# Kernel tuning notes

Hardware: AMD Instinct MI355X
Metric: run time of the kernel (lower is better)

The kernel has to match this reference:

```python
import jax, jax.numpy as jnp
import numpy as np

DIM = 128
HEADS = 4
HD = DIM // HEADS  # 32
WS = 8             # search window (ws x ws candidates)
K = 16             # top-k neighbors kept
SCALE = HD ** -0.5


def _sepconv(x, w_dw, w_pw, b):
    # depthwise 3x3 ('SAME', reflect-free) + pointwise 1x1 with bias (SepConv2d)
    C = x.shape[1]
    y = jax.lax.conv_general_dilated(x, w_dw, (1, 1), 'SAME',
                                     feature_group_count=C,
                                     dimension_numbers=('NCHW', 'OIHW', 'NCHW'))
    return jnp.einsum('bchw,oc->bohw', y, w_pw) + b[None, :, None, None]


def _refl(i, n):
    # dnls reflect_bounds: mirror indices back into [0, n-1]
    i = jnp.where(i < 0, -i, i)
    return jnp.where(i >= n, 2 * (n - 1) - i, i)


def _neighbor_idx(T, H, W, ws):
    # flat pixel index of the ws*ws spatial candidates per query (wt=0: same frame)
    off = jnp.arange(ws) - ws // 2
    ni = _refl(jnp.arange(H)[:, None] + off[None, :], H)  # [H,ws]
    nj = _refl(jnp.arange(W)[:, None] + off[None, :], W)  # [W,ws]
    pix = ni[:, None, :, None] * W + nj[None, :, None, :]  # [H,W,ws,ws]
    idx = jnp.arange(T)[:, None, None, None, None] * (H * W) + pix[None]
    return idx.reshape(T * H * W, ws * ws).astype(jnp.int32)  # [Q,L]


def reference(vid, wq_dw, wq_pw, bq, wk_dw, wk_pw, bk, wv_dw, wv_pw, bv, proj_w, proj_b):
    B, T, C, H, W = vid.shape
    Q = T * H * W
    x = vid.reshape(B * T, C, H, W)
    # qkv conv projection; q pre-scaled as in get_qkv
    q = _sepconv(x, wq_dw, wq_pw, bq) * SCALE
    k = _sepconv(x, wk_dw, wk_pw, bk)
    v = _sepconv(x, wv_dw, wv_pw, bv)

    def heads(z):  # [B*T,C,H,W] -> [B,heads,Q,hd]
        return z.reshape(B, T, HEADS, HD, H, W).transpose(0, 2, 1, 4, 5, 3).reshape(B, HEADS, Q, HD)

    qh, kh, vh = heads(q), heads(k), heads(v)
    idx = _neighbor_idx(T, H, W, WS)            # [Q,L]
    kg = jnp.take(kh, idx, axis=2)              # [B,h,Q,L,hd] irregular gather
    dists = jnp.einsum('bhqd,bhqld->bhql', qh, kg)
    vals, args = jax.lax.top_k(dists, K)        # k-NN by prod distance
    attn = jax.nn.softmax(vals, axis=-1)        # run_softmax over k
    sel = jnp.take_along_axis(jnp.broadcast_to(idx[None, None], (B, HEADS) + idx.shape), args, axis=-1)
    vsel = jnp.take_along_axis(vh, sel.reshape(B, HEADS, Q * K)[..., None], axis=2).reshape(B, HEADS, Q, K, HD)
    out = jnp.einsum('bhqk,bhqkd->bhqd', attn, vsel)   # wpsum (ps=pt=1)
    out = out.transpose(0, 2, 1, 3).reshape(B, Q, C)   # merge heads: (h c)
    y = out @ proj_w.T + proj_b                        # nn.Linear proj
    # fold: ps=1, stride0=1 -> zvid==1, pure reshape back to video
    return y.reshape(B, T, H, W, C).transpose(0, 1, 4, 2, 3)


def setup_inputs() -> dict:
    key = jax.random.key(0)
    ks = jax.random.split(key, 12)
    s = 0.02
    return {
        'vid': jax.random.normal(ks[0], (1, 2, DIM, 96, 96), jnp.float32),
        'wq_dw': jax.random.normal(ks[1], (DIM, 1, 3, 3), jnp.float32) * s,
        'wq_pw': jax.random.normal(ks[2], (DIM, DIM), jnp.float32) * s,
        'bq': jax.random.normal(ks[3], (DIM,), jnp.float32) * s,
        'wk_dw': jax.random.normal(ks[4], (DIM, 1, 3, 3), jnp.float32) * s,
        'wk_pw': jax.random.normal(ks[5], (DIM, DIM), jnp.float32) * s,
        'bk': jax.random.normal(ks[6], (DIM,), jnp.float32) * s,
        'wv_dw': jax.random.normal(ks[7], (DIM, 1, 3, 3), jnp.float32) * s,
        'wv_pw': jax.random.normal(ks[8], (DIM, DIM), jnp.float32) * s,
        'bv': jax.random.normal(ks[9], (DIM,), jnp.float32) * s,
        'proj_w': jax.random.normal(ks[10], (DIM, DIM), jnp.float32) * s,
        'proj_b': jax.random.normal(ks[11], (DIM,), jnp.float32) * s,
    }
```

## Files before the change

kernel.cpp:

```cpp
#include <hip/hip_runtime.h>
#include <math.h>

#define TT 2
#define CH 128
#define HH 96
#define WW 96
#define HWS 9216
#define QTOT 18432
#define QC (QTOT*CH)
#define HD 32
#define KTOP 16
#define SCALE 0.17677669529663687f

#define SEG 16
#define PR 8
#define PC 23
#define PSTRIDE 36

#define WB_TOT 98304

typedef __attribute__((ext_vector_type(8))) short short8;
typedef __attribute__((ext_vector_type(4))) float floatx4;

__device__ __forceinline__ unsigned short f2bf(float f) {
    union { float f; unsigned u; } x; x.f = f;
    unsigned r = x.u + 0x7fffu + ((x.u >> 16) & 1u);
    return (unsigned short)(r >> 16);
}
__device__ __forceinline__ float bf2f(unsigned short h) {
    return __uint_as_float(((unsigned)h) << 16);
}

__device__ __forceinline__ int refl(int x, int n) {
    x = x < 0 ? -x : x;
    return x >= n ? 2 * (n - 1) - x : x;
}

__global__ __launch_bounds__(256) void dwcvt_kernel(
    const float* __restrict__ x,
    const float* __restrict__ wq, const float* __restrict__ wk, const float* __restrict__ wv,
    const float* __restrict__ wq_pw, const float* __restrict__ wk_pw,
    const float* __restrict__ wv_pw, const float* __restrict__ proj_w,
    unsigned short* __restrict__ qk_hi,
    unsigned short* __restrict__ qk_lo,
    unsigned short* __restrict__ v_bf,
    unsigned short* __restrict__ wbuf)
{
    int t = threadIdx.x;
    if (blockIdx.x == 288) {
        int y = blockIdx.y;
        const float* src = y == 0 ? wq_pw : (y == 1 ? wk_pw : (y == 2 ? wv_pw : proj_w));
        unsigned short* hi = wbuf + (y == 0 ? 0 : (y == 1 ? 32768 : (y == 2 ? 65536 : 81920)));
#pragma unroll
        for (int r = 0; r < 16; r++) {
            int idx = r * 256 + t;
            float4 w4 = *(const float4*)(src + idx * 4);
            unsigned short hx = f2bf(w4.x), hy = f2bf(w4.y), hz = f2bf(w4.z), hw = f2bf(w4.w);
            uint2 pk;
            pk.x = hx | ((unsigned)hy << 16); pk.y = hz | ((unsigned)hw << 16);
            *(uint2*)(hi + idx * 4) = pk;
            if (y < 2) {
                unsigned short lx = f2bf(w4.x - bf2f(hx)), ly = f2bf(w4.y - bf2f(hy));
                unsigned short lz = f2bf(w4.z - bf2f(hz)), lw = f2bf(w4.w - bf2f(hw));
                pk.x = lx | ((unsigned)ly << 16); pk.y = lz | ((unsigned)lw << 16);
                *(uint2*)(hi + 16384 + idx * 4) = pk;
            }
        }
        return;
    }

    int pl = t & 63;
    int cg = __builtin_amdgcn_readfirstlane(t >> 6);
    int p  = blockIdx.x * 64 + pl;
    int c0 = blockIdx.y * 32 + cg * 8;
    int hw = p % HWS;
    int tt = p / HWS;
    int i = hw / WW, j = hw % WW;

    unsigned qh[4], ql[4], kh[4], kl[4], vh4[4];
#pragma unroll
    for (int ic = 0; ic < 8; ic += 2) {
        float sv[3][2];
#pragma unroll
        for (int u = 0; u < 2; u++) {
            int c = c0 + ic + u;
            const float* xp = x + (size_t)(tt * CH + c) * HWS;
            float w0[9], w1[9], w2[9];
#pragma unroll
            for (int r = 0; r < 9; r++) {
                w0[r] = wq[c * 9 + r]; w1[r] = wk[c * 9 + r]; w2[r] = wv[c * 9 + r];
            }
            float s0 = 0.f, s1 = 0.f, s2 = 0.f;
#pragma unroll
            for (int r = 0; r < 3; r++) {
                int ii = i + r - 1;
                if (ii < 0 || ii >= HH) continue;
#pragma unroll
                for (int ss = 0; ss < 3; ss++) {
                    int jj = j + ss - 1;
                    if (jj < 0 || jj >= WW) continue;
                    float xv = xp[ii * WW + jj];
                    s0 += xv * w0[r * 3 + ss];
                    s1 += xv * w1[r * 3 + ss];
                    s2 += xv * w2[r * 3 + ss];
                }
            }
            sv[0][u] = s0; sv[1][u] = s1; sv[2][u] = s2;
        }
        int w = ic >> 1;
        unsigned short h0 = f2bf(sv[0][0]), h1 = f2bf(sv[0][1]);
        qh[w] = h0 | ((unsigned)h1 << 16);
        ql[w] = f2bf(sv[0][0] - bf2f(h0)) | ((unsigned)f2bf(sv[0][1] - bf2f(h1)) << 16);
        h0 = f2bf(sv[1][0]); h1 = f2bf(sv[1][1]);
        kh[w] = h0 | ((unsigned)h1 << 16);
        kl[w] = f2bf(sv[1][0] - bf2f(h0)) | ((unsigned)f2bf(sv[1][1] - bf2f(h1)) << 16);
        vh4[w] = f2bf(sv[2][0]) | ((unsigned)f2bf(sv[2][1]) << 16);
    }
    size_t off = (size_t)p * CH + c0;
    uint4 pk;
    pk.x = qh[0]; pk.y = qh[1]; pk.z = qh[2]; pk.w = qh[3];
    *(uint4*)(qk_hi + off) = pk;
    pk.x = ql[0]; pk.y = ql[1]; pk.z = ql[2]; pk.w = ql[3];
    *(uint4*)(qk_lo + off) = pk;
    pk.x = kh[0]; pk.y = kh[1]; pk.z = kh[2]; pk.w = kh[3];
    *(uint4*)(qk_hi + (size_t)QC + off) = pk;
    pk.x = kl[0]; pk.y = kl[1]; pk.z = kl[2]; pk.w = kl[3];
    *(uint4*)(qk_lo + (size_t)QC + off) = pk;
    pk.x = vh4[0]; pk.y = vh4[1]; pk.z = vh4[2]; pk.w = vh4[3];
    *(uint4*)(v_bf + off) = pk;
}

__global__ __launch_bounds__(256) void qkv_mfma(
    const unsigned short* __restrict__ Ahi,
    const unsigned short* __restrict__ Alo,
    const unsigned short* __restrict__ Avb,
    const unsigned short* __restrict__ wbuf,
    const float* __restrict__ bq, const float* __restrict__ bk, const float* __restrict__ bv,
    float* __restrict__ qkf,
    unsigned short* __restrict__ vh)
{
    int sel = blockIdx.y;
    int t = threadIdx.x;
    int wv = t >> 6, lane = t & 63;
    int m = lane & 15, quad = lane >> 4;
    int p0 = blockIdx.x * 64;
    int o0 = wv * 32;

    if (sel == 2) {
        const unsigned short* Wg = wbuf + 65536;
        float bb[2];
#pragma unroll
        for (int ot = 0; ot < 2; ot++) bb[ot] = bv[o0 + ot * 16 + m];
        floatx4 acc[4][2];
#pragma unroll
        for (int i = 0; i < 4; i++)
#pragma unroll
            for (int j = 0; j < 2; j++) acc[i][j] = (floatx4){0.f, 0.f, 0.f, 0.f};
#pragma unroll
        for (int kc = 0; kc < 4; kc++) {
            short8 a[4], b[2];
#pragma unroll
            for (int pt = 0; pt < 4; pt++)
                a[pt] = *(const short8*)(Avb + (size_t)(p0 + pt * 16 + m) * CH + kc * 32 + quad * 8);
#pragma unroll
            for (int ot = 0; ot < 2; ot++)
                b[ot] = *(const short8*)(Wg + (size_t)(o0 + ot * 16 + m) * CH + kc * 32 + quad * 8);
#pragma unroll
            for (int pt = 0; pt < 4; pt++)
#pragma unroll
                for (int ot = 0; ot < 2; ot++)
                    acc[pt][ot] = __builtin_amdgcn_mfma_f32_16x16x32_bf16(a[pt], b[ot], acc[pt][ot], 0, 0, 0);
        }
        unsigned short* vhh = vh + (size_t)wv * QTOT * 32;
#pragma unroll
        for (int pt = 0; pt < 4; pt++)
#pragma unroll
            for (int ot = 0; ot < 2; ot++)
#pragma unroll
                for (int reg = 0; reg < 4; reg++) {
                    int p = p0 + pt * 16 + quad * 4 + reg;
                    vhh[(size_t)p * 32 + ot * 16 + m] = f2bf(acc[pt][ot][reg] + bb[ot]);
                }
        return;
    }

    const unsigned short* Wh_g = wbuf + sel * 32768;
    const unsigned short* Wl_g = Wh_g + 16384;
    const float* bias = sel ? bk : bq;
    float scale = sel ? 1.f : SCALE;
    const unsigned short* ah = Ahi + (size_t)sel * QC;
    const unsigned short* al = Alo + (size_t)sel * QC;
    float* O = qkf + (size_t)sel * QC;

    float bb[2];
#pragma unroll
    for (int ot = 0; ot < 2; ot++) bb[ot] = bias[o0 + ot * 16 + m];
    floatx4 acc[4][2];
#pragma unroll
    for (int i = 0; i < 4; i++)
#pragma unroll
        for (int j = 0; j < 2; j++) acc[i][j] = (floatx4){0.f, 0.f, 0.f, 0.f};
#pragma unroll
    for (int kc = 0; kc < 4; kc++) {
        short8 avh[4], avl[4], bh[2], bl[2];
#pragma unroll
        for (int pt = 0; pt < 4; pt++) {
            size_t base = (size_t)(p0 + pt * 16 + m) * CH + kc * 32 + quad * 8;
            avh[pt] = *(const short8*)(ah + base);
            avl[pt] = *(const short8*)(al + base);
        }
#pragma unroll
        for (int ot = 0; ot < 2; ot++) {
            size_t widx = (size_t)(o0 + ot * 16 + m) * CH + kc * 32 + quad * 8;
            bh[ot] = *(const short8*)(Wh_g + widx);
            bl[ot] = *(const short8*)(Wl_g + widx);
        }
#pragma unroll
        for (int pt = 0; pt < 4; pt++)
#pragma unroll
            for (int ot = 0; ot < 2; ot++) {
                acc[pt][ot] = __builtin_amdgcn_mfma_f32_16x16x32_bf16(avh[pt], bh[ot], acc[pt][ot], 0, 0, 0);
                acc[pt][ot] = __builtin_amdgcn_mfma_f32_16x16x32_bf16(avh[pt], bl[ot], acc[pt][ot], 0, 0, 0);
                acc[pt][ot] = __builtin_amdgcn_mfma_f32_16x16x32_bf16(avl[pt], bh[ot], acc[pt][ot], 0, 0, 0);
            }
    }
#pragma unroll
    for (int pt = 0; pt < 4; pt++)
#pragma unroll
        for (int ot = 0; ot < 2; ot++)
#pragma unroll
            for (int reg = 0; reg < 4; reg++) {
                int p = p0 + pt * 16 + quad * 4 + reg;
                O[(size_t)p * CH + o0 + ot * 16 + m] = (acc[pt][ot][reg] + bb[ot]) * scale;
            }
}

__global__ __launch_bounds__(1024) void attn_kernel(
    const float* __restrict__ q,
    const float* __restrict__ k,
    const unsigned short* __restrict__ vh,
    unsigned short* __restrict__ att)
{
    __shared__ float kp[PR * PC * PSTRIDE];
    __shared__ uint2 slot[16][KTOP];
    int h = blockIdx.y;
    int n = blockIdx.x;
    int seg = (n & 7) * 144 + (n >> 3);
    int qj0 = (seg % (WW / SEG)) * SEG;
    int qi = (seg / (WW / SEG)) % HH;
    int tt = seg / ((WW / SEG) * HH);
    int t = threadIdx.x;

#pragma unroll
    for (int r = 0; r < 2; r++) {
        int f = r * 1024 + t;
        if (f < PR * PC * 8) {
            int pix = f >> 3, d4 = f & 7;
            int ci = pix / PC, cj = pix - ci * PC;
            int gi = refl(qi + ci - 4, HH);
            int gj = refl(qj0 + cj - 4, WW);
            int gp = tt * HWS + gi * WW + gj;
            *(float4*)(&kp[pix * PSTRIDE + d4 * 4]) =
                *(const float4*)(k + (size_t)gp * CH + h * HD + d4 * 4);
        }
    }

    int wv = t >> 6, lane = t & 63;
    int wvu = __builtin_amdgcn_readfirstlane(wv);
    if (lane < KTOP) slot[wvu][lane] = make_uint2(0u, 0u);
    __syncthreads();

    int ci = lane >> 3, cjo = lane & 7;
    int di = ci - 4, dj = cjo - 4;
    int rowoff = tt * HWS + refl(qi + di, HH) * WW;
    const unsigned long long below = (1ull << lane) - 1ull;
    const unsigned short* vhh = vh + (size_t)h * QTOT * 32;

    int ql = wvu;
    int qj = qj0 + ql;
    int p = tt * HWS + qi * WW + qj;

    const float* qp = q + (size_t)p * CH + h * HD;
    int pixq = ci * PC + ql + cjo;
    const float* kr = &kp[pixq * PSTRIDE];
    float dist = 0.f;
#pragma unroll
    for (int dd = 0; dd < 8; dd++) {
        float4 qv = *(const float4*)(qp + dd * 4);
        float4 kv = *(const float4*)(kr + dd * 4);
        dist += qv.x * kv.x + qv.y * kv.y + qv.z * kv.z + qv.w * kv.w;
    }

    unsigned u = __float_as_uint(dist);
    unsigned key = (u & 0x80000000u) ? ~u : (u | 0x80000000u);
    unsigned khi = key >> 16, klo = key & 0xffffu;
    float e = __expf(dist);

    unsigned Lh = 0u;
#pragma unroll
    for (int bit = 15; bit >= 0; --bit) {
        unsigned C = Lh | (1u << bit);
        unsigned long long b = __ballot(khi >= C);
        Lh = (__popcll(b) >= KTOP) ? C : Lh;
    }
    bool gth = khi > Lh;
    bool eqh = (khi == Lh);
    unsigned long long gtmh = __ballot(gth);
    unsigned long long eqmh = __ballot(eqh);
    int need = KTOP - __popcll(gtmh);
    bool selb;
    unsigned long long selm;
    if (__popcll(eqmh) == need) {
        selb = gth || eqh;
        selm = gtmh | eqmh;
    } else {
        unsigned Ll = 0u;
#pragma unroll
        for (int bit = 15; bit >= 0; --bit) {
            unsigned C = Ll | (1u << bit);
            unsigned long long b = __ballot(klo >= C) & eqmh;
            Ll = (__popcll(b) >= need) ? C : Ll;
        }
        unsigned long long gtml = __ballot(klo > Ll) & eqmh;
        unsigned long long eqml = __ballot(klo == Ll) & eqmh;
        int needl = need - __popcll(gtml);
        int rk = __popcll(eqml & below);
        bool gtl = eqh && (klo > Ll);
        bool eql = eqh && (klo == Ll);
        selb = gth || gtl || (eql && rk < needl);
        selm = __ballot(selb);
    }
    int rksel = __builtin_amdgcn_mbcnt_hi(
        (unsigned)(selm >> 32), __builtin_amdgcn_mbcnt_lo((unsigned)selm, 0));
    int cpix = rowoff + refl(qj + dj, WW);
    if (selb && rksel < KTOP)
        slot[wvu][rksel] = make_uint2(__float_as_uint(e), (unsigned)(cpix << 5));

    const int d = lane & (HD - 1);
    const int half8 = (lane >> 5) * 8;
    float acc = 0.f, denom = 0.f;
#pragma unroll
    for (int r = 0; r < 8; r++) {
        uint2 sp = slot[wvu][half8 + r];
        float a0 = __uint_as_float(sp.x);
        denom += a0;
        acc += a0 * bf2f(vhh[(size_t)sp.y + d]);
    }
    acc += __shfl_xor(acc, 32);
    denom += __shfl_xor(denom, 32);
    if (lane < HD)
        att[(size_t)p * CH + h * HD + lane] =
            f2bf(acc * __builtin_amdgcn_rcpf(denom));
}

__global__ __launch_bounds__(256) void proj_mfma(
    const unsigned short* __restrict__ A,
    const unsigned short* __restrict__ wbuf,
    const float* __restrict__ bias,
    float* __restrict__ out)
{
    const unsigned short* Wg = wbuf + 81920;
    int t = threadIdx.x;
    int wv = t >> 6, lane = t & 63;
    int m = lane & 15, quad = lane >> 4;
    int p0 = blockIdx.x * 64;
    int o0 = wv * 32;
    float bb[2][4];
#pragma unroll
    for (int ot = 0; ot < 2; ot++)
#pragma unroll
        for (int reg = 0; reg < 4; reg++) bb[ot][reg] = bias[o0 + ot * 16 + quad * 4 + reg];
    floatx4 acc[2][4];
#pragma unroll
    for (int i = 0; i < 2; i++)
#pragma unroll
        for (int j = 0; j < 4; j++) acc[i][j] = (floatx4){0.f, 0.f, 0.f, 0.f};
#pragma unroll
    for (int kc = 0; kc < 4; kc++) {
        short8 a[2], b[4];
#pragma unroll
        for (int ot = 0; ot < 2; ot++)
            a[ot] = *(const short8*)(Wg + (size_t)(o0 + ot * 16 + m) * CH + kc * 32 + quad * 8);
#pragma unroll
        for (int pt = 0; pt < 4; pt++)
            b[pt] = *(const short8*)(A + (size_t)(p0 + pt * 16 + m) * CH + kc * 32 + quad * 8);
#pragma unroll
        for (int ot = 0; ot < 2; ot++)
#pragma unroll
            for (int pt = 0; pt < 4; pt++)
                acc[ot][pt] = __builtin_amdgcn_mfma_f32_16x16x32_bf16(a[ot], b[pt], acc[ot][pt], 0, 0, 0);
    }
    int tt = p0 / HWS;
    int hwb = p0 - tt * HWS;
#pragma unroll
    for (int ot = 0; ot < 2; ot++)
#pragma unroll
        for (int pt = 0; pt < 4; pt++)
#pragma unroll
            for (int reg = 0; reg < 4; reg++) {
                int o = o0 + ot * 16 + quad * 4 + reg;
                int hw = hwb + pt * 16 + m;
                out[((size_t)(tt * CH + o)) * HWS + hw] = acc[ot][pt][reg] + bb[ot][reg];
            }
}

extern "C" void kernel_launch(void* const* d_in, const int* in_sizes, int n_in,
                              void* d_out, int out_size, void* d_ws, size_t ws_size,
                              hipStream_t stream) {
    const float* vid    = (const float*)d_in[0];
    const float* wq_dw  = (const float*)d_in[1];
    const float* wq_pw  = (const float*)d_in[2];
    const float* bq     = (const float*)d_in[3];
    const float* wk_dw  = (const float*)d_in[4];
    const float* wk_pw  = (const float*)d_in[5];
    const float* bk     = (const float*)d_in[6];
    const float* wv_dw  = (const float*)d_in[7];
    const float* wv_pw  = (const float*)d_in[8];
    const float* bv     = (const float*)d_in[9];
    const float* proj_w = (const float*)d_in[10];
    const float* proj_b = (const float*)d_in[11];
    float* out = (float*)d_out;

    float* qkf = (float*)d_ws;
    unsigned short* vh = (unsigned short*)(qkf + (size_t)2 * QC);
    unsigned short* qk_hi = vh + (size_t)QC;
    unsigned short* qk_lo = qk_hi + (size_t)2 * QC;
    unsigned short* v_bf = qk_lo + (size_t)2 * QC;
    unsigned short* wbuf = v_bf + (size_t)QC;
    unsigned short* att_bf = v_bf;

    dwcvt_kernel<<<dim3(289, 4), 256, 0, stream>>>(
        vid, wq_dw, wk_dw, wv_dw, wq_pw, wk_pw, wv_pw, proj_w,
        qk_hi, qk_lo, v_bf, wbuf);
    qkv_mfma<<<dim3(QTOT / 64, 3), 256, 0, stream>>>(
        qk_hi, qk_lo, v_bf, wbuf, bq, bk, bv, qkf, vh);
    attn_kernel<<<dim3(TT * HH * (WW / SEG), 4), 1024, 0, stream>>>(
        qkf, qkf + (size_t)QC, vh, att_bf);
    proj_mfma<<<QTOT / 64, 256, 0, stream>>>(att_bf, wbuf, proj_b, out);
}
```

Baseline: 179.4 us.

## Fuse depthwise conv and QKV pointwise GEMM through shared memory staging

Merges the depthwise-conv/bf16-split kernel and the QKV MFMA kernel into one kernel. The per-pixel hi/lo bf16 activations are staged in LDS instead of being written to and re-read from global buffers. The separate weight pre-conversion pass is removed, and the fp32 pointwise and projection weights are converted to bf16 hi/lo inside the MFMA loops. This drops one launch and a large global round trip. In exchange each block redoes the weight conversion, uses 32-pixel tiles with more LDS, and adds branchless masked conv loads.

```diff
diff --git a/kernel.cpp b/kernel.cpp
--- a/kernel.cpp
+++ b/kernel.cpp
@@ -17,7 +17,7 @@
 #define PC 23
 #define PSTRIDE 36
 
-#define WB_TOT 98304
+#define FPX 32
 
 typedef __attribute__((ext_vector_type(8))) short short8;
 typedef __attribute__((ext_vector_type(4))) float floatx4;
@@ -36,196 +36,149 @@
     return x >= n ? 2 * (n - 1) - x : x;
 }
 
-__global__ __launch_bounds__(256) void dwcvt_kernel(
+__device__ __forceinline__ short8 pack_hi(float4 a, float4 b) {
+    union { unsigned short us[8]; short8 v; } u;
+    u.us[0] = f2bf(a.x); u.us[1] = f2bf(a.y);
+    u.us[2] = f2bf(a.z); u.us[3] = f2bf(a.w);
+    u.us[4] = f2bf(b.x); u.us[5] = f2bf(b.y);
+    u.us[6] = f2bf(b.z); u.us[7] = f2bf(b.w);
+    return u.v;
+}
+__device__ __forceinline__ short8 pack_lo(float4 a, float4 b, short8 hi) {
+    union { unsigned short us[8]; short8 v; } u;
+    u.us[0] = f2bf(a.x - bf2f((unsigned short)hi[0]));
+    u.us[1] = f2bf(a.y - bf2f((unsigned short)hi[1]));
+    u.us[2] = f2bf(a.z - bf2f((unsigned short)hi[2]));
+    u.us[3] = f2bf(a.w - bf2f((unsigned short)hi[3]));
+    u.us[4] = f2bf(b.x - bf2f((unsigned short)hi[4]));
+    u.us[5] = f2bf(b.y - bf2f((unsigned short)hi[5]));
+    u.us[6] = f2bf(b.z - bf2f((unsigned short)hi[6]));
+    u.us[7] = f2bf(b.w - bf2f((unsigned short)hi[7]));
+    return u.v;
+}
+
+__global__ __launch_bounds__(512) void dwqkv_kernel(
     const float* __restrict__ x,
-    const float* __restrict__ wq, const float* __restrict__ wk, const float* __restrict__ wv,
-    const float* __restrict__ wq_pw, const float* __restrict__ wk_pw,
-    const float* __restrict__ wv_pw, const float* __restrict__ proj_w,
-    unsigned short* __restrict__ qk_hi,
-    unsigned short* __restrict__ qk_lo,
-    unsigned short* __restrict__ v_bf,
-    unsigned short* __restrict__ wbuf)
+    const float* __restrict__ wqd, const float* __restrict__ wkd, const float* __restrict__ wvd,
+    const float* __restrict__ wq_pw, const float* __restrict__ wk_pw, const float* __restrict__ wv_pw,
+    const float* __restrict__ bq, const float* __restrict__ bk, const float* __restrict__ bv,
+    float* __restrict__ qkf,
+    unsigned short* __restrict__ vh)
 {
+    __shared__ float wS[3456];
+    __shared__ unsigned short pl[5][FPX * 136];
     int t = threadIdx.x;
-    if (blockIdx.x == 288) {
-        int y = blockIdx.y;
-        const float* src = y == 0 ? wq_pw : (y == 1 ? wk_pw : (y == 2 ? wv_pw : proj_w));
-        unsigned short* hi = wbuf + (y == 0 ? 0 : (y == 1 ? 32768 : (y == 2 ? 65536 : 81920)));
-#pragma unroll
-        for (int r = 0; r < 16; r++) {
-            int idx = r * 256 + t;
-            float4 w4 = *(const float4*)(src + idx * 4);
-            unsigned short hx = f2bf(w4.x), hy = f2bf(w4.y), hz = f2bf(w4.z), hw = f2bf(w4.w);
-            uint2 pk;
-            pk.x = hx | ((unsigned)hy << 16); pk.y = hz | ((unsigned)hw << 16);
-            *(uint2*)(hi + idx * 4) = pk;
-            if (y < 2) {
-                unsigned short lx = f2bf(w4.x - bf2f(hx)), ly = f2bf(w4.y - bf2f(hy));
-                unsigned short lz = f2bf(w4.z - bf2f(hz)), lw = f2bf(w4.w - bf2f(hw));
-                pk.x = lx | ((unsigned)ly << 16); pk.y = lz | ((unsigned)lw << 16);
-                *(uint2*)(hi + 16384 + idx * 4) = pk;
-            }
-        }
-        return;
-    }
-
-    int pl = t & 63;
-    int cg = __builtin_amdgcn_readfirstlane(t >> 6);
-    int p  = blockIdx.x * 64 + pl;
-    int c0 = blockIdx.y * 32 + cg * 8;
-    int hw = p % HWS;
-    int tt = p / HWS;
-    int i = hw / WW, j = hw % WW;
-
-    unsigned qh[4], ql[4], kh[4], kl[4], vh4[4];
+    for (int r = t; r < 1152; r += 512) {
+        wS[r] = wqd[r]; wS[1152 + r] = wkd[r]; wS[2304 + r] = wvd[r];
+    }
+    int p0 = blockIdx.x * FPX;
+    int tt0 = p0 / HWS;
+    int hw0 = p0 - tt0 * HWS;
+    int i0 = hw0 / WW, j0 = hw0 - i0 * WW;
+    int px = t & 31, cgp = t >> 5;
+    int c0 = cgp * 8;
+    int j = j0 + px;
+
+    int off[9]; float mk[9];
+#pragma unroll
+    for (int r = 0; r < 3; r++) {
+        int ii = i0 + r - 1;
+        float rm = (ii >= 0 && ii < HH) ? 1.f : 0.f;
+        int iic = ii < 0 ? 0 : (ii >= HH ? HH - 1 : ii);
+#pragma unroll
+        for (int s = 0; s < 3; s++) {
+            int jj = j + s - 1;
+            float cm = (jj >= 0 && jj < WW) ? 1.f : 0.f;
+            int jjc = jj < 0 ? 0 : (jj >= WW ? WW - 1 : jj);
+            off[r * 3 + s] = iic * WW + jjc;
+            mk[r * 3 + s] = rm * cm;
+        }
+    }
+    __syncthreads();
+
+    unsigned qh[4], ql2[4], kh[4], kl[4], vh4[4];
 #pragma unroll
     for (int ic = 0; ic < 8; ic += 2) {
         float sv[3][2];
 #pragma unroll
         for (int u = 0; u < 2; u++) {
             int c = c0 + ic + u;
-            const float* xp = x + (size_t)(tt * CH + c) * HWS;
-            float w0[9], w1[9], w2[9];
-#pragma unroll
-            for (int r = 0; r < 9; r++) {
-                w0[r] = wq[c * 9 + r]; w1[r] = wk[c * 9 + r]; w2[r] = wv[c * 9 + r];
-            }
+            const float* xp = x + (size_t)(tt0 * CH + c) * HWS;
+            const float* w0 = &wS[c * 9];
+            const float* w1 = &wS[1152 + c * 9];
+            const float* w2 = &wS[2304 + c * 9];
             float s0 = 0.f, s1 = 0.f, s2 = 0.f;
 #pragma unroll
-            for (int r = 0; r < 3; r++) {
-                int ii = i + r - 1;
-                if (ii < 0 || ii >= HH) continue;
-#pragma unroll
-                for (int ss = 0; ss < 3; ss++) {
-                    int jj = j + ss - 1;
-                    if (jj < 0 || jj >= WW) continue;
-                    float xv = xp[ii * WW + jj];
-                    s0 += xv * w0[r * 3 + ss];
-                    s1 += xv * w1[r * 3 + ss];
-                    s2 += xv * w2[r * 3 + ss];
-                }
+            for (int q9 = 0; q9 < 9; q9++) {
+                float xv = xp[off[q9]] * mk[q9];
+                s0 += xv * w0[q9]; s1 += xv * w1[q9]; s2 += xv * w2[q9];
             }
             sv[0][u] = s0; sv[1][u] = s1; sv[2][u] = s2;
         }
         int w = ic >> 1;
         unsigned short h0 = f2bf(sv[0][0]), h1 = f2bf(sv[0][1]);
         qh[w] = h0 | ((unsigned)h1 << 16);
-        ql[w] = f2bf(sv[0][0] - bf2f(h0)) | ((unsigned)f2bf(sv[0][1] - bf2f(h1)) << 16);
+        ql2[w] = f2bf(sv[0][0] - bf2f(h0)) | ((unsigned)f2bf(sv[0][1] - bf2f(h1)) << 16);
         h0 = f2bf(sv[1][0]); h1 = f2bf(sv[1][1]);
         kh[w] = h0 | ((unsigned)h1 << 16);
         kl[w] = f2bf(sv[1][0] - bf2f(h0)) | ((unsigned)f2bf(sv[1][1] - bf2f(h1)) << 16);
         vh4[w] = f2bf(sv[2][0]) | ((unsigned)f2bf(sv[2][1]) << 16);
     }
-    size_t off = (size_t)p * CH + c0;
+    int lb = px * 136 + c0;
     uint4 pk;
-    pk.x = qh[0]; pk.y = qh[1]; pk.z = qh[2]; pk.w = qh[3];
-    *(uint4*)(qk_hi + off) = pk;
-    pk.x = ql[0]; pk.y = ql[1]; pk.z = ql[2]; pk.w = ql[3];
-    *(uint4*)(qk_lo + off) = pk;
-    pk.x = kh[0]; pk.y = kh[1]; pk.z = kh[2]; pk.w = kh[3];
-    *(uint4*)(qk_hi + (size_t)QC + off) = pk;
-    pk.x = kl[0]; pk.y = kl[1]; pk.z = kl[2]; pk.w = kl[3];
-    *(uint4*)(qk_lo + (size_t)QC + off) = pk;
-    pk.x = vh4[0]; pk.y = vh4[1]; pk.z = vh4[2]; pk.w = vh4[3];
-    *(uint4*)(v_bf + off) = pk;
-}
-
-__global__ __launch_bounds__(256) void qkv_mfma(
-    const unsigned short* __restrict__ Ahi,
-    const unsigned short* __restrict__ Alo,
-    const unsigned short* __restrict__ Avb,
-    const unsigned short* __restrict__ wbuf,
-    const float* __restrict__ bq, const float* __restrict__ bk, const float* __restrict__ bv,
-    float* __restrict__ qkf,
-    unsigned short* __restrict__ vh)
-{
-    int sel = blockIdx.y;
-    int t = threadIdx.x;
+    pk.x = qh[0];  pk.y = qh[1];  pk.z = qh[2];  pk.w = qh[3];  *(uint4*)&pl[0][lb] = pk;
+    pk.x = ql2[0]; pk.y = ql2[1]; pk.z = ql2[2]; pk.w = ql2[3]; *(uint4*)&pl[1][lb] = pk;
+    pk.x = kh[0];  pk.y = kh[1];  pk.z = kh[2];  pk.w = kh[3];  *(uint4*)&pl[2][lb] = pk;
+    pk.x = kl[0];  pk.y = kl[1];  pk.z = kl[2];  pk.w = kl[3];  *(uint4*)&pl[3][lb] = pk;
+    pk.x = vh4[0]; pk.y = vh4[1]; pk.z = vh4[2]; pk.w = vh4[3]; *(uint4*)&pl[4][lb] = pk;
+    __syncthreads();
+
     int wv = t >> 6, lane = t & 63;
     int m = lane & 15, quad = lane >> 4;
-    int p0 = blockIdx.x * 64;
-    int o0 = wv * 32;
-
-    if (sel == 2) {
-        const unsigned short* Wg = wbuf + 65536;
-        float bb[2];
-#pragma unroll
-        for (int ot = 0; ot < 2; ot++) bb[ot] = bv[o0 + ot * 16 + m];
-        floatx4 acc[4][2];
-#pragma unroll
-        for (int i = 0; i < 4; i++)
-#pragma unroll
-            for (int j = 0; j < 2; j++) acc[i][j] = (floatx4){0.f, 0.f, 0.f, 0.f};
-#pragma unroll
-        for (int kc = 0; kc < 4; kc++) {
-            short8 a[4], b[2];
-#pragma unroll
-            for (int pt = 0; pt < 4; pt++)
-                a[pt] = *(const short8*)(Avb + (size_t)(p0 + pt * 16 + m) * CH + kc * 32 + quad * 8);
-#pragma unroll
-            for (int ot = 0; ot < 2; ot++)
-                b[ot] = *(const short8*)(Wg + (size_t)(o0 + ot * 16 + m) * CH + kc * 32 + quad * 8);
-#pragma unroll
-            for (int pt = 0; pt < 4; pt++)
-#pragma unroll
-                for (int ot = 0; ot < 2; ot++)
-                    acc[pt][ot] = __builtin_amdgcn_mfma_f32_16x16x32_bf16(a[pt], b[ot], acc[pt][ot], 0, 0, 0);
-        }
-        unsigned short* vhh = vh + (size_t)wv * QTOT * 32;
-#pragma unroll
-        for (int pt = 0; pt < 4; pt++)
-#pragma unroll
-            for (int ot = 0; ot < 2; ot++)
-#pragma unroll
-                for (int reg = 0; reg < 4; reg++) {
-                    int p = p0 + pt * 16 + quad * 4 + reg;
-                    vhh[(size_t)p * 32 + ot * 16 + m] = f2bf(acc[pt][ot][reg] + bb[ot]);
-                }
-        return;
-    }
-
-    const unsigned short* Wh_g = wbuf + sel * 32768;
-    const unsigned short* Wl_g = Wh_g + 16384;
-    const float* bias = sel ? bk : bq;
-    float scale = sel ? 1.f : SCALE;
-    const unsigned short* ah = Ahi + (size_t)sel * QC;
-    const unsigned short* al = Alo + (size_t)sel * QC;
-    float* O = qkf + (size_t)sel * QC;
-
+    int o0 = (wv & 3) * 32;
+    bool isQ = wv < 4;
+    const float* Wf = isQ ? wq_pw : wk_pw;
+    const unsigned short* Ah = pl[isQ ? 0 : 2];
+    const unsigned short* Al = pl[isQ ? 1 : 3];
+    const float* bias = isQ ? bq : bk;
+    float scale = isQ ? SCALE : 1.f;
+    float* O = qkf + (isQ ? 0 : (size_t)QC);
     float bb[2];
 #pragma unroll
     for (int ot = 0; ot < 2; ot++) bb[ot] = bias[o0 + ot * 16 + m];
-    floatx4 acc[4][2];
-#pragma unroll
-    for (int i = 0; i < 4; i++)
-#pragma unroll
-        for (int j = 0; j < 2; j++) acc[i][j] = (floatx4){0.f, 0.f, 0.f, 0.f};
+    floatx4 acc[2][2];
+#pragma unroll
+    for (int i = 0; i < 2; i++)
+#pragma unroll
+        for (int jj2 = 0; jj2 < 2; jj2++) acc[i][jj2] = (floatx4){0.f, 0.f, 0.f, 0.f};
 #pragma unroll
     for (int kc = 0; kc < 4; kc++) {
-        short8 avh[4], avl[4], bh[2], bl[2];
-#pragma unroll
-        for (int pt = 0; pt < 4; pt++) {
-            size_t base = (size_t)(p0 + pt * 16 + m) * CH + kc * 32 + quad * 8;
-            avh[pt] = *(const short8*)(ah + base);
-            avl[pt] = *(const short8*)(al + base);
+        short8 avh[2], avl[2], bh2[2], bl2[2];
+#pragma unroll
+        for (int pt = 0; pt < 2; pt++) {
+            int lidx = (pt * 16 + m) * 136 + kc * 32 + quad * 8;
+            avh[pt] = *(const short8*)&Ah[lidx];
+            avl[pt] = *(const short8*)&Al[lidx];
         }
 #pragma unroll
         for (int ot = 0; ot < 2; ot++) {
-            size_t widx = (size_t)(o0 + ot * 16 + m) * CH + kc * 32 + quad * 8;
-            bh[ot] = *(const short8*)(Wh_g + widx);
-            bl[ot] = *(const short8*)(Wl_g + widx);
-        }
-#pragma unroll
-        for (int pt = 0; pt < 4; pt++)
+            const float* wrow = Wf + (size_t)(o0 + ot * 16 + m) * CH + kc * 32 + quad * 8;
+            float4 wa = *(const float4*)wrow;
+            float4 wb = *(const float4*)(wrow + 4);
+            bh2[ot] = pack_hi(wa, wb);
+            bl2[ot] = pack_lo(wa, wb, bh2[ot]);
+        }
+#pragma unroll
+        for (int pt = 0; pt < 2; pt++)
 #pragma unroll
             for (int ot = 0; ot < 2; ot++) {
-                acc[pt][ot] = __builtin_amdgcn_mfma_f32_16x16x32_bf16(avh[pt], bh[ot], acc[pt][ot], 0, 0, 0);
-                acc[pt][ot] = __builtin_amdgcn_mfma_f32_16x16x32_bf16(avh[pt], bl[ot], acc[pt][ot], 0, 0, 0);
-                acc[pt][ot] = __builtin_amdgcn_mfma_f32_16x16x32_bf16(avl[pt], bh[ot], acc[pt][ot], 0, 0, 0);
+                acc[pt][ot] = __builtin_amdgcn_mfma_f32_16x16x32_bf16(avh[pt], bh2[ot], acc[pt][ot], 0, 0, 0);
+                acc[pt][ot] = __builtin_amdgcn_mfma_f32_16x16x32_bf16(avh[pt], bl2[ot], acc[pt][ot], 0, 0, 0);
+                acc[pt][ot] = __builtin_amdgcn_mfma_f32_16x16x32_bf16(avl[pt], bh2[ot], acc[pt][ot], 0, 0, 0);
             }
     }
 #pragma unroll
-    for (int pt = 0; pt < 4; pt++)
+    for (int pt = 0; pt < 2; pt++)
 #pragma unroll
         for (int ot = 0; ot < 2; ot++)
 #pragma unroll
@@ -233,6 +186,33 @@
                 int p = p0 + pt * 16 + quad * 4 + reg;
                 O[(size_t)p * CH + o0 + ot * 16 + m] = (acc[pt][ot][reg] + bb[ot]) * scale;
             }
+
+    int ptv = wv >> 2;
+    float bbv[2];
+#pragma unroll
+    for (int ot = 0; ot < 2; ot++) bbv[ot] = bv[o0 + ot * 16 + m];
+    floatx4 accv[2];
+    accv[0] = (floatx4){0.f, 0.f, 0.f, 0.f};
+    accv[1] = (floatx4){0.f, 0.f, 0.f, 0.f};
+#pragma unroll
+    for (int kc = 0; kc < 4; kc++) {
+        int lidx = (ptv * 16 + m) * 136 + kc * 32 + quad * 8;
+        short8 av = *(const short8*)&pl[4][lidx];
+#pragma unroll
+        for (int ot = 0; ot < 2; ot++) {
+            const float* wrow = wv_pw + (size_t)(o0 + ot * 16 + m) * CH + kc * 32 + quad * 8;
+            short8 bhv = pack_hi(*(const float4*)wrow, *(const float4*)(wrow + 4));
+            accv[ot] = __builtin_amdgcn_mfma_f32_16x16x32_bf16(av, bhv, accv[ot], 0, 0, 0);
+        }
+    }
+    unsigned short* vhh = vh + (size_t)(wv & 3) * QTOT * 32;
+#pragma unroll
+    for (int ot = 0; ot < 2; ot++)
+#pragma unroll
+        for (int reg = 0; reg < 4; reg++) {
+            int p = p0 + ptv * 16 + quad * 4 + reg;
+            vhh[(size_t)p * 32 + ot * 16 + m] = f2bf(accv[ot][reg] + bbv[ot]);
+        }
 }
 
 __global__ __launch_bounds__(1024) void attn_kernel(
@@ -355,11 +335,10 @@
 
 __global__ __launch_bounds__(256) void proj_mfma(
     const unsigned short* __restrict__ A,
-    const unsigned short* __restrict__ wbuf,
+    const float* __restrict__ proj_w,
     const float* __restrict__ bias,
     float* __restrict__ out)
 {
-    const unsigned short* Wg = wbuf + 81920;
     int t = threadIdx.x;
     int wv = t >> 6, lane = t & 63;
     int m = lane & 15, quad = lane >> 4;
@@ -374,13 +353,15 @@
 #pragma unroll
     for (int i = 0; i < 2; i++)
 #pragma unroll
-        for (int j = 0; j < 4; j++) acc[i][j] = (floatx4){0.f, 0.f, 0.f, 0.f};
+        for (int jj2 = 0; jj2 < 4; jj2++) acc[i][jj2] = (floatx4){0.f, 0.f, 0.f, 0.f};
 #pragma unroll
     for (int kc = 0; kc < 4; kc++) {
         short8 a[2], b[4];
 #pragma unroll
-        for (int ot = 0; ot < 2; ot++)
-            a[ot] = *(const short8*)(Wg + (size_t)(o0 + ot * 16 + m) * CH + kc * 32 + quad * 8);
+        for (int ot = 0; ot < 2; ot++) {
+            const float* wrow = proj_w + (size_t)(o0 + ot * 16 + m) * CH + kc * 32 + quad * 8;
+            a[ot] = pack_hi(*(const float4*)wrow, *(const float4*)(wrow + 4));
+        }
 #pragma unroll
         for (int pt = 0; pt < 4; pt++)
             b[pt] = *(const short8*)(A + (size_t)(p0 + pt * 16 + m) * CH + kc * 32 + quad * 8);
@@ -423,18 +404,11 @@
 
     float* qkf = (float*)d_ws;
     unsigned short* vh = (unsigned short*)(qkf + (size_t)2 * QC);
-    unsigned short* qk_hi = vh + (size_t)QC;
-    unsigned short* qk_lo = qk_hi + (size_t)2 * QC;
-    unsigned short* v_bf = qk_lo + (size_t)2 * QC;
-    unsigned short* wbuf = v_bf + (size_t)QC;
-    unsigned short* att_bf = v_bf;
-
-    dwcvt_kernel<<<dim3(289, 4), 256, 0, stream>>>(
-        vid, wq_dw, wk_dw, wv_dw, wq_pw, wk_pw, wv_pw, proj_w,
-        qk_hi, qk_lo, v_bf, wbuf);
-    qkv_mfma<<<dim3(QTOT / 64, 3), 256, 0, stream>>>(
-        qk_hi, qk_lo, v_bf, wbuf, bq, bk, bv, qkf, vh);
+    unsigned short* att_bf = vh + (size_t)QC;
+
+    dwqkv_kernel<<<QTOT / FPX, 512, 0, stream>>>(
+        vid, wq_dw, wk_dw, wv_dw, wq_pw, wk_pw, wv_pw, bq, bk, bv, qkf, vh);
     attn_kernel<<<dim3(TT * HH * (WW / SEG), 4), 1024, 0, stream>>>(
         qkf, qkf + (size_t)QC, vh, att_bf);
-    proj_mfma<<<QTOT / 64, 256, 0, stream>>>(att_bf, wbuf, proj_b, out);
-}
+    proj_mfma<<<QTOT / 64, 256, 0, stream>>>(att_bf, proj_w, proj_b, out);
+}
```

Result: faster. 167.1 us (-6.9%).
